# Performance work log

Hardware: AMD Instinct MI355X
Metric: run time of the kernel (lower is better)

Reference implementation:

```python
import jax, jax.numpy as jnp
import numpy as np


def _normal_distance(n1, n2):
    # Cosine-style normal distance: 1 - <n1, n2>. The original module stubs
    # this as 0; we use the canonical mesh-normal loss so the cdist+argmin+
    # gather chain is exercised end-to-end.
    return 1.0 - jnp.sum(n1 * n2, axis=-1)


def setup_inputs() -> dict:
    key = jax.random.key(0)
    k1, k2, k3, k4 = jax.random.split(key, 4)
    N, M = 8192, 32768
    pred_pts = jax.random.normal(k1, (1, N, 3), dtype=jnp.float32)
    pred_nrm = jax.random.normal(k2, (1, N, 3), dtype=jnp.float32)
    gt_pts = jax.random.normal(k3, (1, M, 3), dtype=jnp.float32)
    gt_nrm = jax.random.normal(k4, (1, M, 3), dtype=jnp.float32)
    # unit normals, as on a real mesh
    pred_nrm = pred_nrm / jnp.linalg.norm(pred_nrm, axis=-1, keepdims=True)
    gt_nrm = gt_nrm / jnp.linalg.norm(gt_nrm, axis=-1, keepdims=True)
    return {
        "predicted_points_batch": pred_pts,
        "predicted_normals_batch": pred_nrm,
        "gt_points_batch": gt_pts,
        "gt_normals_batch": gt_nrm,
    }


def reference(predicted_points_batch, predicted_normals_batch,
              gt_points_batch, gt_normals_batch):
    # Original forward returns inside the first loop iteration -> element 0 only.
    p = predicted_points_batch[0]    # [N,3]
    pn = predicted_normals_batch[0]  # [N,3]
    g = gt_points_batch[0]           # [M,3]
    gn = gt_normals_batch[0]         # [M,3]

    # Squared pairwise distances (monotone in true cdist; only argmin is used).
    # d2[i,j] = |p_i|^2 + |g_j|^2 - 2 p_i . g_j   -> one [N,M] intermediate.
    d2 = (jnp.sum(p * p, axis=1)[:, None]
          + jnp.sum(g * g, axis=1)[None, :]
          - 2.0 * (p @ g.T))                      # [N,M]

    gt_idx = jnp.argmin(d2, axis=1)    # nearest gt point per predicted point, [N]
    pr_idx = jnp.argmin(d2, axis=0)    # nearest predicted point per gt point, [M]

    nearest_gt_normals = gn[gt_idx]    # [N,3]
    nearest_pr_normals = pn[pr_idx]    # [M,3]

    dist1 = _normal_distance(pn, nearest_gt_normals)  # [N]
    dist2 = _normal_distance(gn, nearest_pr_normals)  # [M]
    return jnp.mean(dist1) + jnp.mean(dist2)
```

## Files before the change

### kernel.cpp

```cpp
#include <hip/hip_runtime.h>
#include <stdint.h>
#include <float.h>

#define BLK 256
#define IPT 8
#define OWNERS (BLK * IPT)
#define SLICE 256
#define SUB 64
#define KROW 64
#define KCOL 32
#define FBLK 64

typedef unsigned long long ull;
typedef float v2f __attribute__((ext_vector_type(2)));

__device__ __forceinline__ v2f fma2(v2f a, v2f b, v2f c) {
    return __builtin_elementwise_fma(a, b, c);
}

__device__ __forceinline__ unsigned int ford(float f) {
    int b = __float_as_int(f);
    return (b >= 0) ? ((unsigned)b ^ 0x80000000u) : ~(unsigned)b;
}
__device__ __forceinline__ float ford_inv(unsigned int u) {
    int b = (u & 0x80000000u) ? (int)(u ^ 0x80000000u) : (int)~u;
    return __int_as_float(b);
}

__global__ __launch_bounds__(BLK) void nn_scan(
    const float* __restrict__ p, const float* __restrict__ g,
    ull* __restrict__ wsR, ull* __restrict__ wsC,
    float* __restrict__ out, int N, int M)
{
    __shared__ float sbx[SLICE], sby[SLICE], sbz[SLICE], sbw[SLICE];

    if (blockIdx.x == 0 && threadIdx.x == 0) *out = 0.0f;

    const int rowChunks = N / OWNERS;
    const int rowBlocks = rowChunks * KROW;

    const float* A; const float* B; ull* ws; int id, nK, NO, cpb;
    if ((int)blockIdx.x < rowBlocks) {
        id = blockIdx.x;             A = p; B = g; ws = wsR; nK = KROW; NO = N; cpb = M / KROW;
    } else {
        id = blockIdx.x - rowBlocks; A = g; B = p; ws = wsC; nK = KCOL; NO = M; cpb = N / KCOL;
    }
    const int chunk = id / nK;
    const int kgrp  = id - chunk * nK;
    const int c0 = kgrp * cpb;
    const int nStages = cpb / SLICE;

    const int o0 = chunk * OWNERS + threadIdx.x;
    v2f ax2[IPT], ay2[IPT], az2[IPT];
    float best[IPT];
    int base[IPT];
#pragma unroll
    for (int r = 0; r < IPT; ++r) {
        int o = o0 + r * BLK;
        float axv = -2.0f * A[3 * o];
        float ayv = -2.0f * A[3 * o + 1];
        float azv = -2.0f * A[3 * o + 2];
        ax2[r] = (v2f){axv, axv};
        ay2[r] = (v2f){ayv, ayv};
        az2[r] = (v2f){azv, azv};
        best[r] = FLT_MAX;
        base[r] = c0;
    }

    for (int stage = 0; stage < nStages; ++stage) {
        const int gs0 = c0 + stage * SLICE;
        if (stage) __syncthreads();

        {
            int s = gs0 + threadIdx.x;
            float bx = B[3 * s], by = B[3 * s + 1], bz = B[3 * s + 2];
            float w = fmaf(bz, bz, fmaf(by, by, bx * bx));
            sbx[threadIdx.x] = bx; sby[threadIdx.x] = by;
            sbz[threadIdx.x] = bz; sbw[threadIdx.x] = w;
        }
        __syncthreads();

        for (int st = 0; st < SLICE; st += SUB) {
            float prev[IPT];
#pragma unroll
            for (int r = 0; r < IPT; ++r) prev[r] = best[r];
#pragma unroll 2
            for (int k = st; k < st + SUB; k += 2) {
                v2f qx = *(const v2f*)&sbx[k];
                v2f qy = *(const v2f*)&sby[k];
                v2f qz = *(const v2f*)&sbz[k];
                v2f qw = *(const v2f*)&sbw[k];
#pragma unroll
                for (int r = 0; r < IPT; ++r) {
                    v2f t = fma2(az2[r], qz, qw);
                    t = fma2(ay2[r], qy, t);
                    t = fma2(ax2[r], qx, t);
                    best[r] = fminf(fminf(t.x, t.y), best[r]);
                }
            }
#pragma unroll
            for (int r = 0; r < IPT; ++r)
                if (best[r] < prev[r]) base[r] = gs0 + st;
        }
    }

    ull* dst = ws + (size_t)kgrp * NO;
#pragma unroll
    for (int r = 0; r < IPT; ++r)
        dst[o0 + r * BLK] = ((ull)ford(best[r]) << 32) | (unsigned)base[r];
}

__global__ __launch_bounds__(FBLK) void nn_reduce(
    const ull* __restrict__ wsR, const ull* __restrict__ wsC,
    const float* __restrict__ p, const float* __restrict__ g,
    const float* __restrict__ pn, const float* __restrict__ gn,
    float* __restrict__ out, int N, int M, float invN, float invM)
{
    int t = blockIdx.x * FBLK + threadIdx.x;
    float c = 0.0f;
    if (t < N + M) {
        const float* A; const float* B; const float* An; const float* Bn;
        const ull* ws; int o, K, NO; float inv;
        if (t < N) { o = t;     A = p; B = g; An = pn; Bn = gn; ws = wsR; K = KROW; NO = N; inv = invN; }
        else       { o = t - N; A = g; B = p; An = gn; Bn = pn; ws = wsC; K = KCOL; NO = M; inv = invM; }

        ull bestp = ws[o];
#pragma unroll 4
        for (int k = 1; k < K; ++k) {
            ull v2 = ws[(size_t)k * NO + o];
            bestp = (v2 < bestp) ? v2 : bestp;
        }

        float ax = -2.0f * A[3 * o];
        float ay = -2.0f * A[3 * o + 1];
        float az = -2.0f * A[3 * o + 2];
        float bestf = ford_inv((unsigned int)(bestp >> 32));
        int b0 = (int)(bestp & 0xffffffffull);

        int idx = 0x7fffffff;
#pragma unroll 4
        for (int jj = 0; jj < SUB; ++jj) {
            int s = b0 + jj;
            float bx = B[3 * s], by = B[3 * s + 1], bz = B[3 * s + 2];
            float w = fmaf(bz, bz, fmaf(by, by, bx * bx));
            float v = fmaf(ax, bx, fmaf(ay, by, fmaf(az, bz, w)));
            int cand = (v == bestf) ? s : 0x7fffffff;
            idx = (cand < idx) ? cand : idx;
        }
        if (idx == 0x7fffffff) idx = b0;

        float d = An[3 * o] * Bn[3 * idx] + An[3 * o + 1] * Bn[3 * idx + 1]
                + An[3 * o + 2] * Bn[3 * idx + 2];
        c = (1.0f - d) * inv;
    }
#pragma unroll
    for (int off = 32; off > 0; off >>= 1) c += __shfl_down(c, off, 64);
    if (threadIdx.x == 0) atomicAdd(out, c);
}

#define L_SLICE 128

__global__ __launch_bounds__(BLK) void nn_min_dual(
    const float* __restrict__ p, const float* __restrict__ g,
    ull* __restrict__ rowmin, ull* __restrict__ colmin,
    float* __restrict__ out, int rowBlocks, int rowSlices, int colSlices)
{
    __shared__ float sbx[L_SLICE], sby[L_SLICE], sbz[L_SLICE], sbw[L_SLICE];
    if (blockIdx.x == 0 && threadIdx.x == 0) *out = 0.0f;
    const float* A; const float* B; ull* outmin; int id, nSlices;
    if ((int)blockIdx.x < rowBlocks) {
        id = blockIdx.x;             A = p; B = g; outmin = rowmin; nSlices = rowSlices;
    } else {
        id = blockIdx.x - rowBlocks; A = g; B = p; outmin = colmin; nSlices = colSlices;
    }
    const int chunk = id / nSlices;
    const int slice = id - chunk * nSlices;
    const int s0 = slice * L_SLICE;
    if (threadIdx.x < L_SLICE) {
        int s = s0 + threadIdx.x;
        float bx = B[3 * s], by = B[3 * s + 1], bz = B[3 * s + 2];
        float w = fmaf(bz, bz, fmaf(by, by, bx * bx));
        sbx[threadIdx.x] = bx; sby[threadIdx.x] = by;
        sbz[threadIdx.x] = bz; sbw[threadIdx.x] = w;
    }
    const int o0 = chunk * OWNERS + threadIdx.x;
    v2f ax2[IPT], ay2[IPT], az2[IPT];
    float best[IPT]; int base[IPT];
#pragma unroll
    for (int r = 0; r < IPT; ++r) {
        int o = o0 + r * BLK;
        float axv = -2.0f * A[3 * o], ayv = -2.0f * A[3 * o + 1], azv = -2.0f * A[3 * o + 2];
        ax2[r] = (v2f){axv, axv}; ay2[r] = (v2f){ayv, ayv}; az2[r] = (v2f){azv, azv};
        best[r] = FLT_MAX; base[r] = s0;
    }
    __syncthreads();
    for (int st = 0; st < L_SLICE; st += SUB) {
        float prev[IPT];
#pragma unroll
        for (int r = 0; r < IPT; ++r) prev[r] = best[r];
#pragma unroll 2
        for (int k = st; k < st + SUB; k += 2) {
            v2f qx = *(const v2f*)&sbx[k]; v2f qy = *(const v2f*)&sby[k];
            v2f qz = *(const v2f*)&sbz[k]; v2f qw = *(const v2f*)&sbw[k];
#pragma unroll
            for (int r = 0; r < IPT; ++r) {
                v2f t = fma2(az2[r], qz, qw);
                t = fma2(ay2[r], qy, t);
                t = fma2(ax2[r], qx, t);
                best[r] = fminf(fminf(t.x, t.y), best[r]);
            }
        }
#pragma unroll
        for (int r = 0; r < IPT; ++r)
            if (best[r] < prev[r]) base[r] = s0 + st;
    }
#pragma unroll
    for (int r = 0; r < IPT; ++r) {
        ull packed = ((ull)ford(best[r]) << 32) | (unsigned)base[r];
        atomicMin(&outmin[o0 + r * BLK], packed);
    }
}

__global__ __launch_bounds__(FBLK) void finalize_legacy(
    const ull* __restrict__ rowmin, const ull* __restrict__ colmin,
    const float* __restrict__ p, const float* __restrict__ g,
    const float* __restrict__ pn, const float* __restrict__ gn,
    float* __restrict__ out, int N, int M, float invN, float invM)
{
    int t = blockIdx.x * FBLK + threadIdx.x;
    float c = 0.0f;
    if (t < N + M) {
        const float* A; const float* B; const float* An; const float* Bn;
        ull packed; int o; float inv;
        if (t < N) { o = t;     A = p; B = g; An = pn; Bn = gn; packed = rowmin[o]; inv = invN; }
        else       { o = t - N; A = g; B = p; An = gn; Bn = pn; packed = colmin[o]; inv = invM; }
        float ax = -2.0f * A[3 * o], ay = -2.0f * A[3 * o + 1], az = -2.0f * A[3 * o + 2];
        float bestf = ford_inv((unsigned int)(packed >> 32));
        int b0 = (int)(packed & 0xffffffffull);
        int idx = 0x7fffffff;
#pragma unroll 4
        for (int jj = 0; jj < SUB; ++jj) {
            int s = b0 + jj;
            float bx = B[3 * s], by = B[3 * s + 1], bz = B[3 * s + 2];
            float w = fmaf(bz, bz, fmaf(by, by, bx * bx));
            float v = fmaf(ax, bx, fmaf(ay, by, fmaf(az, bz, w)));
            int cand = (v == bestf) ? s : 0x7fffffff;
            idx = (cand < idx) ? cand : idx;
        }
        if (idx == 0x7fffffff) idx = b0;
        float d = An[3 * o] * Bn[3 * idx] + An[3 * o + 1] * Bn[3 * idx + 1]
                + An[3 * o + 2] * Bn[3 * idx + 2];
        c = (1.0f - d) * inv;
    }
#pragma unroll
    for (int off = 32; off > 0; off >>= 1) c += __shfl_down(c, off, 64);
    if (threadIdx.x == 0) atomicAdd(out, c);
}

extern "C" void kernel_launch(void* const* d_in, const int* in_sizes, int n_in,
                              void* d_out, int out_size, void* d_ws, size_t ws_size,
                              hipStream_t stream) {
    const float* p  = (const float*)d_in[0];
    const float* pn = (const float*)d_in[1];
    const float* g  = (const float*)d_in[2];
    const float* gn = (const float*)d_in[3];
    const int N = in_sizes[0] / 3;
    const int M = in_sizes[2] / 3;
    float* out = (float*)d_out;

    const size_t wsRn = (size_t)KROW * N;
    const size_t wsCn = (size_t)KCOL * M;
    const size_t needBytes = (wsRn + wsCn) * sizeof(ull);

    const bool geomOK = (N % OWNERS) == 0 && (M % OWNERS) == 0 &&
                        (M % (KROW * SLICE)) == 0 && (N % (KCOL * SLICE)) == 0 &&
                        ((N + M) % FBLK) == 0 && (N % FBLK) == 0;

    if (geomOK && ws_size >= needBytes) {
        ull* wsR = (ull*)d_ws;
        ull* wsC = wsR + wsRn;
        const int blocks = (N / OWNERS) * KROW + (M / OWNERS) * KCOL;
        nn_scan<<<blocks, BLK, 0, stream>>>(p, g, wsR, wsC, out, N, M);
        nn_reduce<<<(N + M) / FBLK, FBLK, 0, stream>>>(
            wsR, wsC, p, g, pn, gn, out, N, M, 1.0f / N, 1.0f / M);
    } else {
        ull* rowmin = (ull*)d_ws;
        ull* colmin = rowmin + N;
        hipMemsetAsync(d_ws, 0xFF, (size_t)(N + M) * sizeof(ull), stream);
        const int rowSlices = M / L_SLICE;
        const int colSlices = N / L_SLICE;
        const int rowBlocks = (N / OWNERS) * rowSlices;
        const int colBlocks = (M / OWNERS) * colSlices;
        nn_min_dual<<<rowBlocks + colBlocks, BLK, 0, stream>>>(
            p, g, rowmin, colmin, out, rowBlocks, rowSlices, colSlices);
        finalize_legacy<<<(N + M + FBLK - 1) / FBLK, FBLK, 0, stream>>>(
            rowmin, colmin, p, g, pn, gn, out, N, M, 1.0f / N, 1.0f / M);
    }
}
```

Measured before the change: 120.7 us.

## Drop per-subslice index tracking, widen register tile, rescan winning chunk in reduce

The scan kernel no longer tracks which 64-wide sub-slice produced each minimum. It stores only the order-mapped 32-bit min per k-group, which halves workspace traffic and removes the prev/base compare bookkeeping from the hot loop. Each thread now owns 16 points instead of 8, with smaller slices and more k-groups, and the launch bounds request 3 waves per SIMD. The reduce kernel recovers the argmin by picking the winning k-group and rescanning its whole chunk (cpb = 256 or 128 points) instead of 64. That shifts work onto the reduce, and the doubled register tile risks spills.

```diff
diff --git a/kernel.cpp b/kernel.cpp
--- a/kernel.cpp
+++ b/kernel.cpp
@@ -3,15 +3,15 @@
 #include <float.h>
 
 #define BLK 256
-#define IPT 8
+#define IPT 16
 #define OWNERS (BLK * IPT)
-#define SLICE 256
-#define SUB 64
-#define KROW 64
-#define KCOL 32
+#define SLICE 128
+#define KROW 128
+#define KCOL 64
 #define FBLK 64
 
 typedef unsigned long long ull;
+typedef unsigned int u32;
 typedef float v2f __attribute__((ext_vector_type(2)));
 
 __device__ __forceinline__ v2f fma2(v2f a, v2f b, v2f c) {
@@ -27,9 +27,9 @@
     return __int_as_float(b);
 }
 
-__global__ __launch_bounds__(BLK) void nn_scan(
-    const float* __restrict__ p, const float* __restrict__ g,
-    ull* __restrict__ wsR, ull* __restrict__ wsC,
+__global__ __launch_bounds__(BLK, 3) void nn_scan(
+    const float* __restrict__ p, const float* __restrict__ g,
+    u32* __restrict__ wsR, u32* __restrict__ wsC,
     float* __restrict__ out, int N, int M)
 {
     __shared__ float sbx[SLICE], sby[SLICE], sbz[SLICE], sbw[SLICE];
@@ -39,7 +39,7 @@
     const int rowChunks = N / OWNERS;
     const int rowBlocks = rowChunks * KROW;
 
-    const float* A; const float* B; ull* ws; int id, nK, NO, cpb;
+    const float* A; const float* B; u32* ws; int id, nK, NO, cpb;
     if ((int)blockIdx.x < rowBlocks) {
         id = blockIdx.x;             A = p; B = g; ws = wsR; nK = KROW; NO = N; cpb = M / KROW;
     } else {
@@ -53,7 +53,6 @@
     const int o0 = chunk * OWNERS + threadIdx.x;
     v2f ax2[IPT], ay2[IPT], az2[IPT];
     float best[IPT];
-    int base[IPT];
 #pragma unroll
     for (int r = 0; r < IPT; ++r) {
         int o = o0 + r * BLK;
@@ -64,14 +63,13 @@
         ay2[r] = (v2f){ayv, ayv};
         az2[r] = (v2f){azv, azv};
         best[r] = FLT_MAX;
-        base[r] = c0;
     }
 
     for (int stage = 0; stage < nStages; ++stage) {
         const int gs0 = c0 + stage * SLICE;
         if (stage) __syncthreads();
 
-        {
+        if (threadIdx.x < SLICE) {
             int s = gs0 + threadIdx.x;
             float bx = B[3 * s], by = B[3 * s + 1], bz = B[3 * s + 2];
             float w = fmaf(bz, bz, fmaf(by, by, bx * bx));
@@ -80,38 +78,30 @@
         }
         __syncthreads();
 
-        for (int st = 0; st < SLICE; st += SUB) {
-            float prev[IPT];
-#pragma unroll
-            for (int r = 0; r < IPT; ++r) prev[r] = best[r];
 #pragma unroll 2
-            for (int k = st; k < st + SUB; k += 2) {
-                v2f qx = *(const v2f*)&sbx[k];
-                v2f qy = *(const v2f*)&sby[k];
-                v2f qz = *(const v2f*)&sbz[k];
-                v2f qw = *(const v2f*)&sbw[k];
-#pragma unroll
-                for (int r = 0; r < IPT; ++r) {
-                    v2f t = fma2(az2[r], qz, qw);
-                    t = fma2(ay2[r], qy, t);
-                    t = fma2(ax2[r], qx, t);
-                    best[r] = fminf(fminf(t.x, t.y), best[r]);
-                }
+        for (int k = 0; k < SLICE; k += 2) {
+            v2f qx = *(const v2f*)&sbx[k];
+            v2f qy = *(const v2f*)&sby[k];
+            v2f qz = *(const v2f*)&sbz[k];
+            v2f qw = *(const v2f*)&sbw[k];
+#pragma unroll
+            for (int r = 0; r < IPT; ++r) {
+                v2f t = fma2(az2[r], qz, qw);
+                t = fma2(ay2[r], qy, t);
+                t = fma2(ax2[r], qx, t);
+                best[r] = fminf(fminf(t.x, t.y), best[r]);
             }
-#pragma unroll
-            for (int r = 0; r < IPT; ++r)
-                if (best[r] < prev[r]) base[r] = gs0 + st;
-        }
-    }
-
-    ull* dst = ws + (size_t)kgrp * NO;
+        }
+    }
+
+    u32* dst = ws + (size_t)kgrp * NO;
 #pragma unroll
     for (int r = 0; r < IPT; ++r)
-        dst[o0 + r * BLK] = ((ull)ford(best[r]) << 32) | (unsigned)base[r];
+        dst[o0 + r * BLK] = ford(best[r]);
 }
 
 __global__ __launch_bounds__(FBLK) void nn_reduce(
-    const ull* __restrict__ wsR, const ull* __restrict__ wsC,
+    const u32* __restrict__ wsR, const u32* __restrict__ wsC,
     const float* __restrict__ p, const float* __restrict__ g,
     const float* __restrict__ pn, const float* __restrict__ gn,
     float* __restrict__ out, int N, int M, float invN, float invM)
@@ -120,27 +110,31 @@
     float c = 0.0f;
     if (t < N + M) {
         const float* A; const float* B; const float* An; const float* Bn;
-        const ull* ws; int o, K, NO; float inv;
-        if (t < N) { o = t;     A = p; B = g; An = pn; Bn = gn; ws = wsR; K = KROW; NO = N; inv = invN; }
-        else       { o = t - N; A = g; B = p; An = gn; Bn = pn; ws = wsC; K = KCOL; NO = M; inv = invM; }
-
-        ull bestp = ws[o];
+        const u32* ws; int o, K, NO, cpb; float inv;
+        if (t < N) { o = t;     A = p; B = g; An = pn; Bn = gn; ws = wsR;
+                     K = KROW; NO = N; cpb = M / KROW; inv = invN; }
+        else       { o = t - N; A = g; B = p; An = gn; Bn = pn; ws = wsC;
+                     K = KCOL; NO = M; cpb = N / KCOL; inv = invM; }
+
+        u32 bestv = ws[o];
+        int bestk = 0;
 #pragma unroll 4
         for (int k = 1; k < K; ++k) {
-            ull v2 = ws[(size_t)k * NO + o];
-            bestp = (v2 < bestp) ? v2 : bestp;
+            u32 v = ws[(size_t)k * NO + o];
+            bestk = (v < bestv) ? k : bestk;
+            bestv = (v < bestv) ? v : bestv;
         }
 
         float ax = -2.0f * A[3 * o];
         float ay = -2.0f * A[3 * o + 1];
         float az = -2.0f * A[3 * o + 2];
-        float bestf = ford_inv((unsigned int)(bestp >> 32));
-        int b0 = (int)(bestp & 0xffffffffull);
+        float bestf = ford_inv(bestv);
+        int b0 = bestk * cpb;
 
         int idx = 0x7fffffff;
 #pragma unroll 4
-        for (int jj = 0; jj < SUB; ++jj) {
-            int s = b0 + jj;
+        for (int j = 0; j < cpb; ++j) {
+            int s = b0 + j;
             float bx = B[3 * s], by = B[3 * s + 1], bz = B[3 * s + 2];
             float w = fmaf(bz, bz, fmaf(by, by, bx * bx));
             float v = fmaf(ax, bx, fmaf(ay, by, fmaf(az, bz, w)));
@@ -158,7 +152,10 @@
     if (threadIdx.x == 0) atomicAdd(out, c);
 }
 
+#define L_IPT 8
+#define L_OWNERS (BLK * L_IPT)
 #define L_SLICE 128
+#define L_SUB 64
 
 __global__ __launch_bounds__(BLK) void nn_min_dual(
     const float* __restrict__ p, const float* __restrict__ g,
@@ -183,27 +180,27 @@
         sbx[threadIdx.x] = bx; sby[threadIdx.x] = by;
         sbz[threadIdx.x] = bz; sbw[threadIdx.x] = w;
     }
-    const int o0 = chunk * OWNERS + threadIdx.x;
-    v2f ax2[IPT], ay2[IPT], az2[IPT];
-    float best[IPT]; int base[IPT];
-#pragma unroll
-    for (int r = 0; r < IPT; ++r) {
+    const int o0 = chunk * L_OWNERS + threadIdx.x;
+    v2f ax2[L_IPT], ay2[L_IPT], az2[L_IPT];
+    float best[L_IPT]; int base[L_IPT];
+#pragma unroll
+    for (int r = 0; r < L_IPT; ++r) {
         int o = o0 + r * BLK;
         float axv = -2.0f * A[3 * o], ayv = -2.0f * A[3 * o + 1], azv = -2.0f * A[3 * o + 2];
         ax2[r] = (v2f){axv, axv}; ay2[r] = (v2f){ayv, ayv}; az2[r] = (v2f){azv, azv};
         best[r] = FLT_MAX; base[r] = s0;
     }
     __syncthreads();
-    for (int st = 0; st < L_SLICE; st += SUB) {
-        float prev[IPT];
-#pragma unroll
-        for (int r = 0; r < IPT; ++r) prev[r] = best[r];
+    for (int st = 0; st < L_SLICE; st += L_SUB) {
+        float prev[L_IPT];
+#pragma unroll
+        for (int r = 0; r < L_IPT; ++r) prev[r] = best[r];
 #pragma unroll 2
-        for (int k = st; k < st + SUB; k += 2) {
+        for (int k = st; k < st + L_SUB; k += 2) {
             v2f qx = *(const v2f*)&sbx[k]; v2f qy = *(const v2f*)&sby[k];
             v2f qz = *(const v2f*)&sbz[k]; v2f qw = *(const v2f*)&sbw[k];
 #pragma unroll
-            for (int r = 0; r < IPT; ++r) {
+            for (int r = 0; r < L_IPT; ++r) {
                 v2f t = fma2(az2[r], qz, qw);
                 t = fma2(ay2[r], qy, t);
                 t = fma2(ax2[r], qx, t);
@@ -211,11 +208,11 @@
             }
         }
 #pragma unroll
-        for (int r = 0; r < IPT; ++r)
+        for (int r = 0; r < L_IPT; ++r)
             if (best[r] < prev[r]) base[r] = s0 + st;
     }
 #pragma unroll
-    for (int r = 0; r < IPT; ++r) {
+    for (int r = 0; r < L_IPT; ++r) {
         ull packed = ((ull)ford(best[r]) << 32) | (unsigned)base[r];
         atomicMin(&outmin[o0 + r * BLK], packed);
     }
@@ -239,7 +236,7 @@
         int b0 = (int)(packed & 0xffffffffull);
         int idx = 0x7fffffff;
 #pragma unroll 4
-        for (int jj = 0; jj < SUB; ++jj) {
+        for (int jj = 0; jj < L_SUB; ++jj) {
             int s = b0 + jj;
             float bx = B[3 * s], by = B[3 * s + 1], bz = B[3 * s + 2];
             float w = fmaf(bz, bz, fmaf(by, by, bx * bx));
@@ -270,15 +267,15 @@
 
     const size_t wsRn = (size_t)KROW * N;
     const size_t wsCn = (size_t)KCOL * M;
-    const size_t needBytes = (wsRn + wsCn) * sizeof(ull);
+    const size_t needBytes = (wsRn + wsCn) * sizeof(u32);
 
     const bool geomOK = (N % OWNERS) == 0 && (M % OWNERS) == 0 &&
                         (M % (KROW * SLICE)) == 0 && (N % (KCOL * SLICE)) == 0 &&
                         ((N + M) % FBLK) == 0 && (N % FBLK) == 0;
 
     if (geomOK && ws_size >= needBytes) {
-        ull* wsR = (ull*)d_ws;
-        ull* wsC = wsR + wsRn;
+        u32* wsR = (u32*)d_ws;
+        u32* wsC = wsR + wsRn;
         const int blocks = (N / OWNERS) * KROW + (M / OWNERS) * KCOL;
         nn_scan<<<blocks, BLK, 0, stream>>>(p, g, wsR, wsC, out, N, M);
         nn_reduce<<<(N + M) / FBLK, FBLK, 0, stream>>>(
@@ -289,8 +286,8 @@
         hipMemsetAsync(d_ws, 0xFF, (size_t)(N + M) * sizeof(ull), stream);
         const int rowSlices = M / L_SLICE;
         const int colSlices = N / L_SLICE;
-        const int rowBlocks = (N / OWNERS) * rowSlices;
-        const int colBlocks = (M / OWNERS) * colSlices;
+        const int rowBlocks = (N / L_OWNERS) * rowSlices;
+        const int colBlocks = (M / L_OWNERS) * colSlices;
         nn_min_dual<<<rowBlocks + colBlocks, BLK, 0, stream>>>(
             p, g, rowmin, colmin, out, rowBlocks, rowSlices, colSlices);
         finalize_legacy<<<(N + M + FBLK - 1) / FBLK, FBLK, 0, stream>>>(
```

Result: slower. 137.6 us (+14.0%).
